# Kernel optimization log

Measured on AMD Instinct MI355X. Metric: run time of the kernel, lower is better.

## Reference

```python
import jax, jax.numpy as jnp
import numpy as np
from jax import lax

ALPHA = 1.0
BETA = 2.0
NUM_ANTS = 16384
NUM_NODES = 512
BATCH = 4096


def setup_inputs() -> dict:
    key = jax.random.key(0)
    k1, k2, k3 = jax.random.split(key, 3)
    x = jax.random.normal(k1, (BATCH, NUM_NODES), dtype=jnp.float32)
    # matches nn.Parameter(torch.ones(N,N)*0.1)
    pheromone_trails = jnp.ones((NUM_NODES, NUM_NODES), dtype=jnp.float32) * 0.1
    # matches nn.Parameter(torch.rand(N,N)*0.1)
    heuristic_info = jax.random.uniform(k2, (NUM_NODES, NUM_NODES), dtype=jnp.float32) * 0.1
    # matches register_buffer('ant_positions', randint(0, N, (num_ants,)))
    ant_positions = jax.random.randint(k3, (NUM_ANTS,), 0, NUM_NODES, dtype=jnp.int32)
    return {"x": x, "pheromone_trails": pheromone_trails,
            "heuristic_info": heuristic_info, "ant_positions": ant_positions}


def reference(x, pheromone_trails, heuristic_info, ant_positions):
    A, N = NUM_ANTS, NUM_NODES
    ant_ids = jnp.arange(A)

    # NOTE: the torch code's select_next_node always reads the row of the ant's
    # *initial* position (self.ant_positions is never updated inside forward),
    # so the unmasked scores are constant per ant. We replicate that faithfully.
    base = (pheromone_trails[ant_positions] ** ALPHA) * \
           (heuristic_info[ant_positions] ** BETA)          # [A, N]

    visited0 = jnp.zeros((A, N), dtype=bool).at[ant_ids, ant_positions].set(True)
    plen0 = jnp.zeros((A,), dtype=jnp.float32)

    def step(carry, _):
        key, visited, current, plen = carry
        key, sub = jax.random.split(key)
        # torch sets masked entries to 0 (NOT -inf) before softmax; replicate.
        logits = jnp.where(visited, 0.0, base)               # [A, N]
        # categorical == multinomial(softmax(logits), 1), vectorized over ants
        nxt = jax.random.categorical(sub, logits, axis=-1)   # [A] int
        plen = plen + heuristic_info[current, nxt]
        visited = visited.at[ant_ids, nxt].set(True)
        return (key, visited, nxt, plen), nxt

    carry0 = (jax.random.key(42), visited0, ant_positions.astype(jnp.int32), plen0)
    (_, _, _, path_lengths), sampled = lax.scan(step, carry0, None, length=N - 1)

    # full paths: [A, N] = start node followed by N-1 sampled nodes
    paths = jnp.concatenate([ant_positions[:, None].astype(sampled.dtype),
                             sampled.T], axis=1)
    # sequential 'if path_length < best' with strict < keeps the FIRST minimum,
    # which is exactly jnp.argmin
    best_idx = jnp.argmin(path_lengths)
    best_path = paths[best_idx].astype(jnp.float32)          # [N]
    return jnp.broadcast_to(best_path[None, :], (x.shape[0], N))
```

## Files before the change

### kernel.cpp

```cpp
#include <hip/hip_runtime.h>
#include <cstdint>
#include <cstddef>

#define A_NUM_ANTS   16384
#define N_NODES      512
#define N_STEPS      511
#define N_BATCH      4096

constexpr uint32_t rotl32(uint32_t x, int r) { return (x << r) | (x >> (32 - r)); }

constexpr void tf2x32(uint32_t k0, uint32_t k1, uint32_t x0, uint32_t x1,
                      uint32_t& o0, uint32_t& o1) {
  const uint32_t k2 = k0 ^ k1 ^ 0x1BD11BDAu;
  x0 += k0; x1 += k1;
  x0 += x1; x1 = rotl32(x1, 13); x1 ^= x0;
  x0 += x1; x1 = rotl32(x1, 15); x1 ^= x0;
  x0 += x1; x1 = rotl32(x1, 26); x1 ^= x0;
  x0 += x1; x1 = rotl32(x1,  6); x1 ^= x0;
  x0 += k1; x1 += k2 + 1u;
  x0 += x1; x1 = rotl32(x1, 17); x1 ^= x0;
  x0 += x1; x1 = rotl32(x1, 29); x1 ^= x0;
  x0 += x1; x1 = rotl32(x1, 16); x1 ^= x0;
  x0 += x1; x1 = rotl32(x1, 24); x1 ^= x0;
  x0 += k2; x1 += k0 + 2u;
  x0 += x1; x1 = rotl32(x1, 13); x1 ^= x0;
  x0 += x1; x1 = rotl32(x1, 15); x1 ^= x0;
  x0 += x1; x1 = rotl32(x1, 26); x1 ^= x0;
  x0 += x1; x1 = rotl32(x1,  6); x1 ^= x0;
  x0 += k0; x1 += k1 + 3u;
  x0 += x1; x1 = rotl32(x1, 17); x1 ^= x0;
  x0 += x1; x1 = rotl32(x1, 29); x1 ^= x0;
  x0 += x1; x1 = rotl32(x1, 16); x1 ^= x0;
  x0 += x1; x1 = rotl32(x1, 24); x1 ^= x0;
  x0 += k1; x1 += k2 + 4u;
  x0 += x1; x1 = rotl32(x1, 13); x1 ^= x0;
  x0 += x1; x1 = rotl32(x1, 15); x1 ^= x0;
  x0 += x1; x1 = rotl32(x1, 26); x1 ^= x0;
  x0 += x1; x1 = rotl32(x1,  6); x1 ^= x0;
  x0 += k2; x1 += k0 + 5u;
  o0 = x0; o1 = x1;
}

struct Subkeys { uint32_t k0[N_STEPS]; uint32_t k1[N_STEPS]; };

constexpr Subkeys make_subkeys() {
  Subkeys s{};
  uint32_t c0 = 0u, c1 = 42u;
  for (int t = 0; t < N_STEPS; ++t) {
    uint32_t n0 = 0, n1 = 0, s0 = 0, s1 = 0;
    tf2x32(c0, c1, 0u, 0u, n0, n1);
    tf2x32(c0, c1, 0u, 1u, s0, s1);
    s.k0[t] = s0; s.k1[t] = s1;
    c0 = n0; c1 = n1;
  }
  return s;
}

namespace { constexpr Subkeys H_SUBKEYS = make_subkeys(); }
__device__ __constant__ Subkeys SUBKEYS = H_SUBKEYS;

#define F32_TINY  1.17549435e-38f
#define NEG_LN2   (-0.69314718056f)

template <bool WRITE_PATH>
__device__ __forceinline__ void simulate_ant(
    int a, int lane,
    const float* __restrict__ pher,
    const float* __restrict__ heur,
    int pos,
    float* __restrict__ plen_out,
    float* __restrict__ path_out)
{
  float lm[8];
  {
    const float* hrow = heur + (size_t)pos * N_NODES;
    const float* prow = pher + (size_t)pos * N_NODES;
#pragma unroll
    for (int q = 0; q < 8; ++q) {
      const int n = lane * 8 + q;
      const float hv = hrow[n];
      const float base = prow[n] * (hv * hv);
      lm[q] = NEG_LN2 * expf(-base);
      if (n == pos) lm[q] = NEG_LN2;
    }
  }

  int   cur  = pos;
  float plen = 0.0f;
  if (WRITE_PATH && lane == 0) path_out[0] = (float)pos;

  const uint32_t ctr_base = (uint32_t)(a * N_NODES + lane * 8);

  for (int t = 0; t < N_STEPS; ++t) {
    const uint32_t k0 = SUBKEYS.k0[t];
    const uint32_t k1 = SUBKEYS.k1[t];

    float bs = 3.4e38f;
    int   bn = 0;
#pragma unroll
    for (int q = 0; q < 8; ++q) {
      uint32_t o0, o1;
      tf2x32(k0, k1, 0u, ctr_base + (uint32_t)q, o0, o1);
      const uint32_t bits = o0 ^ o1;
      const float f = __uint_as_float((bits >> 9) | 0x3f800000u) - 1.0f;
      const float u = fmaxf(f, F32_TINY);
      const float s = __log2f(u) * lm[q];
      const int n = lane * 8 + q;
      if (q == 0 || s < bs) { bs = s; bn = n; }
    }
#pragma unroll
    for (int off = 32; off >= 1; off >>= 1) {
      const float so = __shfl_xor(bs, off, 64);
      const int   no = __shfl_xor(bn, off, 64);
      if (so < bs || (so == bs && no < bn)) { bs = so; bn = no; }
    }
#pragma unroll
    for (int q = 0; q < 8; ++q)
      if (lane * 8 + q == bn) lm[q] = NEG_LN2;

    if (lane == 0) {
      plen += heur[(size_t)cur * N_NODES + bn];
      cur = bn;
      if (WRITE_PATH) path_out[t + 1] = (float)bn;
    }
  }

  if (!WRITE_PATH && lane == 0) plen_out[a] = plen;
}

__global__ __launch_bounds__(256) void aco_sim_kernel(
    const float* __restrict__ pher, const float* __restrict__ heur,
    const int* __restrict__ pos0, float* __restrict__ plen_out, int num_ants)
{
  const int a = (int)((blockIdx.x * blockDim.x + threadIdx.x) >> 6);
  const int lane = threadIdx.x & 63;
  if (a >= num_ants) return;
  simulate_ant<false>(a, lane, pher, heur, pos0[a], plen_out, nullptr);
}

__global__ void aco_argmin_kernel(const float* __restrict__ plen,
                                  int* __restrict__ best, int num_ants) {
  const int tid = threadIdx.x;
  float bv = 3.4e38f;
  int   bi = 0;
  bool  have = false;
  for (int i = tid; i < num_ants; i += 256) {
    const float v = plen[i];
    if (!have || v < bv) { bv = v; bi = i; have = true; }
  }
#pragma unroll
  for (int off = 32; off >= 1; off >>= 1) {
    const float vo = __shfl_xor(bv, off, 64);
    const int   io = __shfl_xor(bi, off, 64);
    if (vo < bv || (vo == bv && io < bi)) { bv = vo; bi = io; }
  }
  __shared__ float sv[4];
  __shared__ int   si[4];
  const int w = tid >> 6;
  if ((tid & 63) == 0) { sv[w] = bv; si[w] = bi; }
  __syncthreads();
  if (tid == 0) {
    for (int j = 1; j < 4; ++j)
      if (sv[j] < bv || (sv[j] == bv && si[j] < bi)) { bv = sv[j]; bi = si[j]; }
    bi = bi < 0 ? 0 : (bi >= num_ants ? num_ants - 1 : bi);
    *best = bi;
  }
}

__global__ void aco_resim_kernel(const float* __restrict__ pher,
                                 const float* __restrict__ heur,
                                 const int* __restrict__ pos0,
                                 const int* __restrict__ best,
                                 float* __restrict__ path_out, int num_ants) {
  const int lane = threadIdx.x & 63;
  int a = *best;
  a = a < 0 ? 0 : (a >= num_ants ? num_ants - 1 : a);
  simulate_ant<true>(a, lane, pher, heur, pos0[a], nullptr, path_out);
}

__global__ void aco_bcast_kernel(float* __restrict__ out, int total4) {
  const int j = (int)(blockIdx.x * blockDim.x + threadIdx.x);
  if (j >= total4) return;
  const int row  = 1 + (j >> 7);
  const int col4 = j & 127;
  const float4 v = reinterpret_cast<const float4*>(out)[col4];
  reinterpret_cast<float4*>(out)[row * 128 + col4] = v;
}

extern "C" void kernel_launch(void* const* d_in, const int* in_sizes, int n_in,
                              void* d_out, int out_size, void* d_ws, size_t ws_size,
                              hipStream_t stream) {
  const float* pher = (const float*)d_in[1];
  const float* heur = (const float*)d_in[2];
  const int*   pos  = (const int*)d_in[3];
  float* out = (float*)d_out;
  const int num_ants = in_sizes[3];

  float* plen = out;
  int*   best = (int*)(out + A_NUM_ANTS);

  const int sim_blocks = (num_ants * 64 + 255) / 256;
  aco_sim_kernel<<<dim3(sim_blocks), dim3(256), 0, stream>>>(
      pher, heur, pos, plen, num_ants);
  aco_argmin_kernel<<<dim3(1), dim3(256), 0, stream>>>(plen, best, num_ants);
  aco_resim_kernel<<<dim3(1), dim3(64), 0, stream>>>(
      pher, heur, pos, best, out, num_ants);
  const int total4 = (out_size - N_NODES) / 4;
  aco_bcast_kernel<<<dim3((total4 + 255) / 256), dim3(256), 0, stream>>>(
      out, total4);
}
```

Measured before the change: 9.324 ms.

## Replace paired shuffle argmin with float-only bpermute min plus ballot winner lookup

The per-step cross-lane argmin now reduces only the float score with ds_bpermute and fminf, using precomputed lane addresses. The winning index is then recovered with a ballot and one shuffle, which takes the lowest lane and lowest q among tied minima. All lanes now do the plen accumulation redundantly instead of branching on lane 0. The fmaxf clamp of the uniform to FLT_MIN is dropped, and launch bounds ask for 6 waves per SIMD. Dropping the clamp lets log2(0) give -inf, which can change sampling when the uniform is exactly zero, and a higher occupancy target may force register spills.

```diff
diff --git a/kernel.cpp b/kernel.cpp
--- a/kernel.cpp
+++ b/kernel.cpp
@@ -59,7 +59,6 @@
 namespace { constexpr Subkeys H_SUBKEYS = make_subkeys(); }
 __device__ __constant__ Subkeys SUBKEYS = H_SUBKEYS;
 
-#define F32_TINY  1.17549435e-38f
 #define NEG_LN2   (-0.69314718056f)
 
 template <bool WRITE_PATH>
@@ -85,50 +84,58 @@
     }
   }
 
+  int baddr[6];
+#pragma unroll
+  for (int r = 0; r < 6; ++r) baddr[r] = ((lane ^ (1 << r)) << 2);
+
   int   cur  = pos;
   float plen = 0.0f;
   if (WRITE_PATH && lane == 0) path_out[0] = (float)pos;
 
   const uint32_t ctr_base = (uint32_t)(a * N_NODES + lane * 8);
+  const int lane8 = lane * 8;
 
   for (int t = 0; t < N_STEPS; ++t) {
     const uint32_t k0 = SUBKEYS.k0[t];
     const uint32_t k1 = SUBKEYS.k1[t];
 
-    float bs = 3.4e38f;
-    int   bn = 0;
+    float s[8];
 #pragma unroll
     for (int q = 0; q < 8; ++q) {
       uint32_t o0, o1;
       tf2x32(k0, k1, 0u, ctr_base + (uint32_t)q, o0, o1);
       const uint32_t bits = o0 ^ o1;
       const float f = __uint_as_float((bits >> 9) | 0x3f800000u) - 1.0f;
-      const float u = fmaxf(f, F32_TINY);
-      const float s = __log2f(u) * lm[q];
-      const int n = lane * 8 + q;
-      if (q == 0 || s < bs) { bs = s; bn = n; }
+      s[q] = __log2f(f) * lm[q];
     }
-#pragma unroll
-    for (int off = 32; off >= 1; off >>= 1) {
-      const float so = __shfl_xor(bs, off, 64);
-      const int   no = __shfl_xor(bn, off, 64);
-      if (so < bs || (so == bs && no < bn)) { bs = so; bn = no; }
+    float smin = s[0];
+#pragma unroll
+    for (int q = 1; q < 8; ++q) smin = fminf(smin, s[q]);
+#pragma unroll
+    for (int r = 0; r < 6; ++r) {
+      const int other = __builtin_amdgcn_ds_bpermute(baddr[r], __float_as_int(smin));
+      smin = fminf(smin, __int_as_float(other));
     }
+    int fq = 8;
+#pragma unroll
+    for (int q = 7; q >= 0; --q) if (s[q] == smin) fq = q;
+    const unsigned long long mask = __ballot(fq < 8);
+    const int winlane = __builtin_ctzll(mask);
+    const int bn = __shfl(fq, winlane, 64) + winlane * 8;
+
 #pragma unroll
     for (int q = 0; q < 8; ++q)
-      if (lane * 8 + q == bn) lm[q] = NEG_LN2;
-
-    if (lane == 0) {
-      plen += heur[(size_t)cur * N_NODES + bn];
-      cur = bn;
-      if (WRITE_PATH) path_out[t + 1] = (float)bn;
-    }
+      if (lane8 + q == bn) lm[q] = NEG_LN2;
+
+    plen += heur[(size_t)cur * N_NODES + bn];
+    cur = bn;
+    if (WRITE_PATH && lane == 0) path_out[t + 1] = (float)bn;
   }
 
   if (!WRITE_PATH && lane == 0) plen_out[a] = plen;
 }
 
-__global__ __launch_bounds__(256) void aco_sim_kernel(
+__global__ __launch_bounds__(256, 6) void aco_sim_kernel(
     const float* __restrict__ pher, const float* __restrict__ heur,
     const int* __restrict__ pos0, float* __restrict__ plen_out, int num_ants)
 {
```

Result: faster. 8.845 ms (-5.1%).
